# Performance work log

Hardware: AMD Instinct MI355X
Metric: run time of the kernel (lower is better)

The kernel has to match this reference:

```python
import jax, jax.numpy as jnp
import numpy as np

B, T, D = 2, 4096, 1024      # batch, seq, hidden_dim
E, I = 16, 512               # n_routed_experts, expert_intermediate
K = 2                        # n_activated_experts
IS = 2048                    # shared_expert_intermediate
ALPHA = 1e-4                 # balance_loss_alpha
EPS = 1e-9


def setup_inputs() -> dict:
    key = jax.random.key(0)
    ks = jax.random.split(key, 8)
    s = lambda k, shape, fan: jax.random.normal(k, shape, jnp.float32) * (fan ** -0.5)
    return {
        "x": jax.random.normal(ks[0], (B, T, D), jnp.float32),
        "gate_w": s(ks[1], (D, E), D),            # router gate (no bias)
        "expert_bias": jnp.zeros((E,), jnp.float32),
        "sh_gate": s(ks[2], (D, IS), D),          # shared expert SwiGLU
        "sh_up": s(ks[3], (D, IS), D),
        "sh_down": s(ks[4], (IS, D), IS),
        "ex_gate": s(ks[5], (E, D, I), D),        # routed experts (stacked)
        "ex_up": s(ks[6], (E, D, I), D),
        "ex_down": s(ks[7], (E, I, D), I),
    }


def _swiglu(x, wg, wu, wd):
    return (jax.nn.silu(x @ wg) * (x @ wu)) @ wd


def reference(x, gate_w, expert_bias, sh_gate, sh_up, sh_down, ex_gate, ex_up, ex_down):
    Bq, Tq, Dq = x.shape
    # shared expert path (n_shared_experts = 1)
    shared = _swiglu(x, sh_gate, sh_up, sh_down)

    xf = x.reshape(Bq * Tq, Dq)                       # (N, D)
    N = xf.shape[0]

    # --- router: sigmoid gating, bias-adjusted top-k, normalized gates ---
    affinity = jax.nn.sigmoid(xf @ gate_w)            # (N, E)
    scores = affinity + expert_bias[None, :]
    _, idx = jax.lax.top_k(scores, K)                 # (N, K) int
    gv = jnp.take_along_axis(affinity, idx, axis=1)   # (N, K) gathered from affinity
    gv = gv / (gv.sum(-1, keepdims=True) + EPS)

    # --- balance loss (sequence-wise, Eq. 17-20) ---
    expert_mask = jax.nn.one_hot(idx, E, dtype=jnp.float32).sum(1)  # (N, E)
    f = expert_mask.sum(0) * E / (K * N)
    P = (affinity / (affinity.sum(-1, keepdims=True) + EPS)).mean(0)
    balance_loss = ALPHA * (f * P).sum()
    expert_counts = expert_mask.sum(0).astype(jnp.int32)            # (E,)

    # --- dispatch/compute/combine, expressed as dense combine-weight matrix ---
    # w[n, e] = sum of gate values for token n routed to expert e (same math
    # as the masked gather/scatter loop in the original)
    w = jnp.zeros((N, E), jnp.float32).at[jnp.arange(N)[:, None], idx].add(gv)
    h = jax.nn.silu(jnp.einsum('nd,edi->eni', xf, ex_gate)) \
        * jnp.einsum('nd,edi->eni', xf, ex_up)        # (E, N, I)
    routed = jnp.einsum('ne,eni,eid->nd', w, h, ex_down)  # (N, D)
    routed = routed.reshape(Bq, Tq, Dq)

    output = shared + routed  # note: original does NOT add residual despite docstring
    return output, balance_loss, expert_counts
```

## Files before the change

kernel.cpp:

```cpp
#include <hip/hip_runtime.h>
#include <stdint.h>

#define NTOK 8192
#define DDIM 1024
#define NEXP 16
#define KSEL 2
#define ISH 2048
#define IEX 512
#define ALPHAC 1e-4f
#define REPS 1e-9f

typedef __attribute__((ext_vector_type(8))) short short8;
typedef __attribute__((ext_vector_type(4))) float f32x4;

__device__ __forceinline__ unsigned short f2bf(float f){
  union { float f; uint32_t u; } v; v.f = f;
  uint32_t u = v.u;
  uint32_t r = (u + 0x7fffu + ((u >> 16) & 1u)) >> 16;
  return (unsigned short)r;
}
__device__ __forceinline__ float bf2f(unsigned short h){
  union { uint32_t u; float f; } v; v.u = ((uint32_t)h) << 16; return v.f;
}

__device__ __forceinline__ void gload16(const void* g, void* l){
  __builtin_amdgcn_global_load_lds(
      (const __attribute__((address_space(1))) void*)g,
      (__attribute__((address_space(3))) void*)l, 16, 0, 0);
}

template<int RM, int RO>
__global__ __launch_bounds__(256) void transpose_bf16(const float* __restrict__ in,
                                                      unsigned short* __restrict__ outp,
                                                      int R, int C){
  __shared__ float tile[64][65];
  const float* ip = in + (size_t)blockIdx.z * R * C;
  unsigned short* op = outp + (size_t)blockIdx.z * R * C * RM;
  int c0 = blockIdx.x * 64, r0 = blockIdx.y * 64;
  int t = threadIdx.x;
  int tr = t >> 4, tc = (t & 15) * 4;
  #pragma unroll
  for (int i = 0; i < 4; ++i){
    float4 v = *(const float4*)&ip[(size_t)(r0 + tr + i*16) * C + c0 + tc];
    tile[tr + i*16][tc+0] = v.x;
    tile[tr + i*16][tc+1] = v.y;
    tile[tr + i*16][tc+2] = v.z;
    tile[tr + i*16][tc+3] = v.w;
  }
  __syncthreads();
  #pragma unroll
  for (int i = 0; i < 4; ++i){
    int oc = tr + i*16;
    ushort4 w;
    w.x = f2bf(tile[tc+0][oc]);
    w.y = f2bf(tile[tc+1][oc]);
    w.z = f2bf(tile[tc+2][oc]);
    w.w = f2bf(tile[tc+3][oc]);
    *(ushort4*)&op[(size_t)((c0 + oc) * RM + RO) * R + r0 + tc] = w;
  }
}

__global__ __launch_bounds__(256) void logits_kernel(
    const float* __restrict__ x, const float* __restrict__ gw,
    float* __restrict__ logits, unsigned short* __restrict__ xb)
{
  __shared__ float gws[16][1024];
  const int t = threadIdx.x;
  #pragma unroll
  for (int k = 0; k < 16; ++k){
    int idx = t + k * 256;
    float4 v = ((const float4*)gw)[idx];
    int d = idx >> 2, e0 = (idx & 3) * 4;
    gws[e0+0][d] = v.x;
    gws[e0+1][d] = v.y;
    gws[e0+2][d] = v.z;
    gws[e0+3][d] = v.w;
  }
  __syncthreads();
  const int lane = t & 63, w = t >> 6;
  const int nb = blockIdx.x * 16 + w * 4;
  for (int i = 0; i < 4; ++i){
    const int n = nb + i;
    const float4* xr = (const float4*)(x + (size_t)n * DDIM);
    ushort4* xo = (ushort4*)(xb + (size_t)n * DDIM);
    float4 xv[4];
    #pragma unroll
    for (int k = 0; k < 4; ++k) xv[k] = xr[lane + k*64];
    #pragma unroll
    for (int k = 0; k < 4; ++k){
      ushort4 ob;
      ob.x = f2bf(xv[k].x); ob.y = f2bf(xv[k].y);
      ob.z = f2bf(xv[k].z); ob.w = f2bf(xv[k].w);
      xo[lane + k*64] = ob;
    }
    float acc[16];
    #pragma unroll
    for (int e = 0; e < 16; ++e){
      float s = 0.f;
      #pragma unroll
      for (int k = 0; k < 4; ++k){
        float4 g = *(const float4*)&gws[e][(lane + k*64)*4];
        s = fmaf(xv[k].x, g.x, fmaf(xv[k].y, g.y, fmaf(xv[k].z, g.z, fmaf(xv[k].w, g.w, s))));
      }
      acc[e] = s;
    }
    #pragma unroll
    for (int m = 1; m < 64; m <<= 1)
      #pragma unroll
      for (int e = 0; e < 16; ++e)
        acc[e] += __shfl_xor(acc[e], m);
    if (lane == 0){
      float4* op = (float4*)(logits + (size_t)n * 16);
      op[0] = make_float4(acc[0],  acc[1],  acc[2],  acc[3]);
      op[1] = make_float4(acc[4],  acc[5],  acc[6],  acc[7]);
      op[2] = make_float4(acc[8],  acc[9],  acc[10], acc[11]);
      op[3] = make_float4(acc[12], acc[13], acc[14], acc[15]);
    }
  }
}

__global__ __launch_bounds__(256) void router_finish(
    const float* __restrict__ logits, const float* __restrict__ ebias,
    int* __restrict__ idxb, float* __restrict__ gvb,
    float* __restrict__ Ppart, int* __restrict__ Cpart)
{
  __shared__ float Ps[16];
  __shared__ int Cs[16];
  const int t = threadIdx.x;
  if (t < 16){ Ps[t] = 0.f; Cs[t] = 0; }
  __syncthreads();
  const int lane = t & 63;
  const int n = blockIdx.x * 256 + t;
  const float4* lp = (const float4*)(logits + (size_t)n * 16);
  float4 a0 = lp[0], a1 = lp[1], a2 = lp[2], a3 = lp[3];
  float aff[16];
  aff[0]=a0.x; aff[1]=a0.y; aff[2]=a0.z; aff[3]=a0.w;
  aff[4]=a1.x; aff[5]=a1.y; aff[6]=a1.z; aff[7]=a1.w;
  aff[8]=a2.x; aff[9]=a2.y; aff[10]=a2.z; aff[11]=a2.w;
  aff[12]=a3.x; aff[13]=a3.y; aff[14]=a3.z; aff[15]=a3.w;
  float rowsum = REPS;
  #pragma unroll
  for (int e = 0; e < 16; ++e){
    aff[e] = 1.f / (1.f + __expf(-aff[e]));
    rowsum += aff[e];
  }
  float bj[16];
  #pragma unroll
  for (int e = 0; e < 16; ++e) bj[e] = ebias[e];
  float bestS = aff[0] + bj[0], bestA = aff[0]; int i1 = 0;
  #pragma unroll
  for (int j = 1; j < 16; ++j){
    float sc = aff[j] + bj[j];
    bool gt2 = sc > bestS;
    bestS = gt2 ? sc : bestS; bestA = gt2 ? aff[j] : bestA; i1 = gt2 ? j : i1;
  }
  float secS = -1e30f, secA = 0.f; int i2 = 0;
  #pragma unroll
  for (int j = 0; j < 16; ++j){
    float sc = aff[j] + bj[j];
    bool ok = (j != i1) && (sc > secS);
    secS = ok ? sc : secS; secA = ok ? aff[j] : secA; i2 = ok ? j : i2;
  }
  float den = bestA + secA + REPS;
  idxb[n*2]   = i1; idxb[n*2+1] = i2;
  gvb[n*2]    = bestA / den; gvb[n*2+1] = secA / den;

  float inv = 1.f / rowsum;
  float pv[16]; int cv[16];
  #pragma unroll
  for (int e = 0; e < 16; ++e){
    pv[e] = aff[e] * inv;
    cv[e] = (e == i1) + (e == i2);
  }
  #pragma unroll
  for (int m = 1; m < 64; m <<= 1)
    #pragma unroll
    for (int e = 0; e < 16; ++e){
      pv[e] += __shfl_xor(pv[e], m);
      cv[e] += __shfl_xor(cv[e], m);
    }
  if (lane == 0){
    #pragma unroll
    for (int e = 0; e < 16; ++e){
      atomicAdd(&Ps[e], pv[e]);
      atomicAdd(&Cs[e], cv[e]);
    }
  }
  __syncthreads();
  if (t < 16){ Ppart[blockIdx.x*16 + t] = Ps[t]; Cpart[blockIdx.x*16 + t] = Cs[t]; }
}

__global__ __launch_bounds__(256) void finalize2(
    const float* __restrict__ Ppart, const int* __restrict__ Cpart,
    int* __restrict__ counts, int* __restrict__ offs, int* __restrict__ cursor,
    float* __restrict__ out_tail)
{
  __shared__ float P[16];
  __shared__ int C[16];
  int t = threadIdx.x;
  if (t < 16){ P[t] = 0.f; C[t] = 0; }
  __syncthreads();
  if (t < 32){
    int e = t & 15, c = t >> 4;
    float p = 0.f; int cc = 0;
    for (int b = c * 16; b < c * 16 + 16; ++b){ p += Ppart[b*16 + e]; cc += Cpart[b*16 + e]; }
    atomicAdd(&P[e], p); atomicAdd(&C[e], cc);
  }
  __syncthreads();
  if (t == 0){
    int a = 0; float loss = 0.f;
    for (int i = 0; i < 16; ++i){
      offs[i] = a; cursor[i] = a; counts[i] = C[i]; a += C[i];
      loss += ((float)C[i] * (float)NEXP / (float)(KSEL * NTOK)) * (P[i] / (float)NTOK);
      out_tail[1+i] = (float)C[i];
    }
    out_tail[0] = ALPHAC * loss;
  }
}

__global__ __launch_bounds__(256) void slot_assign(
    const int* __restrict__ idxb, const float* __restrict__ gvb,
    int* __restrict__ cursor, int* __restrict__ tokp, float* __restrict__ gatep,
    int* __restrict__ rslot)
{
  int i = blockIdx.x * 256 + threadIdx.x;
  int e = idxb[i];
  int s = atomicAdd(&cursor[e], 1);
  tokp[s] = i >> 1;
  gatep[s] = gvb[i];
  rslot[i] = s;
}

template<bool GROUPED, bool GATHER, int MODE, int NYT>
__global__ __launch_bounds__(256) void gemm128(
    const unsigned short* __restrict__ A,
    const unsigned short* __restrict__ B,
    void* __restrict__ Cout,
    int M, int N, int K,
    const int* __restrict__ counts,
    const int* __restrict__ offsets,
    const int* __restrict__ perm,
    const float* __restrict__ rowscale,
    const unsigned short* __restrict__ yb)
{
  __shared__ __align__(16) unsigned short As[128*64];
  __shared__ __align__(16) unsigned short Bs[128*64];

  const int nwg = gridDim.x;
  const int bid = blockIdx.x;
  const int wg = (bid & 7) * (nwg >> 3) + (bid >> 3);
  const int mtl = wg / NYT;
  const int nt  = wg % NYT;

  int mt = mtl, off = 0, cnt = M;
  const unsigned short* bp = B;
  if (GROUPED){
    int acc_ = 0, e = -1;
    #pragma unroll
    for (int i = 0; i < NEXP; ++i){
      int c = counts[i]; int tt = (c + 127) >> 7;
      if (e < 0 && mtl < acc_ + tt){ e = i; mt = mtl - acc_; off = offsets[i]; cnt = c; }
      acc_ += tt;
    }
    if (e < 0) return;
    bp += (size_t)e * N * K;
  }
  const int m0 = mt * 128, n0 = nt * 128;
  const int t = threadIdx.x;
  const int lane = t & 63;
  const int wid = t >> 6;
  const int wm = (wid >> 1) * 64;
  const int wn = (wid & 1) * 64;
  const int l15 = lane & 15, g = lane >> 4;

  const unsigned short* asrc[4];
  const unsigned short* bsrc[4];
  int ldso[4];
  #pragma unroll
  for (int c = 0; c < 4; ++c){
    int s = (wid*4 + c)*64 + lane;
    int row = s >> 3, c16 = s & 7;
    int scol = (c16 ^ (row & 7)) * 8;
    ldso[c] = (wid*4 + c) * 512;
    int r = m0 + row;
    int rc = GROUPED ? (r < cnt ? r : (cnt > 0 ? cnt - 1 : 0)) : r;
    int ar;
    if (GATHER) ar = perm[off + rc];
    else        ar = GROUPED ? off + rc : rc;
    asrc[c] = A + (size_t)ar * K + scol;
    bsrc[c] = bp + (size_t)(n0 + row) * K + scol;
  }

  f32x4 acc[4][4];
  #pragma unroll
  for (int i = 0; i < 4; ++i)
    #pragma unroll
    for (int j = 0; j < 4; ++j)
      #pragma unroll
      for (int r = 0; r < 4; ++r) acc[i][j][r] = 0.f;

  const int ntk = K >> 6;
  for (int tk = 0; tk < ntk; ++tk){
    const int k0 = tk << 6;
    #pragma unroll
    for (int c = 0; c < 4; ++c) gload16(asrc[c] + k0, (void*)&As[ldso[c]]);
    #pragma unroll
    for (int c = 0; c < 4; ++c) gload16(bsrc[c] + k0, (void*)&Bs[ldso[c]]);
    __syncthreads();
    #pragma unroll
    for (int ks = 0; ks < 2; ++ks){
      short8 af[4], bf[4];
      #pragma unroll
      for (int i = 0; i < 4; ++i){
        int row = wm + i * 16 + l15;
        af[i] = *(const short8*)&As[row * 64 + (((ks*4 + g) ^ (row & 7)) * 8)];
      }
      #pragma unroll
      for (int j = 0; j < 4; ++j){
        int row = wn + j * 16 + l15;
        bf[j] = *(const short8*)&Bs[row * 64 + (((ks*4 + g) ^ (row & 7)) * 8)];
      }
      #pragma unroll
      for (int i = 0; i < 4; ++i)
        #pragma unroll
        for (int j = 0; j < 4; ++j)
          acc[i][j] = __builtin_amdgcn_mfma_f32_16x16x32_bf16(af[i], bf[j], acc[i][j], 0, 0, 0);
    }
    __syncthreads();
  }

  #pragma unroll
  for (int i = 0; i < 4; ++i)
    #pragma unroll
    for (int j = 0; j < 4; ++j)
      #pragma unroll
      for (int r = 0; r < 4; ++r){
        int lr = wm + i * 16 + g * 4 + r;
        int grow = m0 + lr;
        if (GROUPED && grow >= cnt) continue;
        int gcol = n0 + wn + j * 16 + l15;
        size_t orow = GROUPED ? (size_t)(off + grow) : (size_t)grow;
        float val = acc[i][j][r];
        if (MODE == 1){
          ((float*)Cout)[orow * N + gcol] = val;
        } else if (MODE == 2){
          val *= rowscale[off + grow];
          ((unsigned short*)Cout)[orow * N + gcol] = f2bf(val);
        } else if (MODE == 6){
          float uo = __shfl_xor(val, 1);
          if (!(l15 & 1)){
            float rv = val / (1.f + __expf(-val)) * uo;
            ((unsigned short*)Cout)[orow * (N >> 1) + (gcol >> 1)] = f2bf(rv);
          }
        } else if (MODE == 7){
          int s0 = perm[grow*2], s1 = perm[grow*2+1];
          float add = bf2f(yb[(size_t)s0 * N + gcol]) + bf2f(yb[(size_t)s1 * N + gcol]);
          ((float*)Cout)[orow * N + gcol] = val + add;
        }
      }
}

template<int MODE, int NYT>
__global__ __launch_bounds__(512, 1) void gemm256(
    const unsigned short* __restrict__ A,
    const unsigned short* __restrict__ B,
    void* __restrict__ Cout,
    int M, int N, int K)
{
  __shared__ __align__(16) unsigned short As[2][256*64];
  __shared__ __align__(16) unsigned short Bs[2][256*64];

  const int nwg = gridDim.x;
  const int bid = blockIdx.x;
  const int wg = (bid & 7) * (nwg >> 3) + (bid >> 3);
  const int mt  = wg / NYT;
  const int ntc = wg % NYT;

  const int m0 = mt * 256, n0 = ntc * 256;
  const int t = threadIdx.x;
  const int lane = t & 63;
  const int wid = t >> 6;
  const int wm0 = (wid >> 2) * 128;
  const int wn0 = (wid & 3) * 64;
  const int l15 = lane & 15, g = lane >> 4;

  const unsigned short* asrc[4];
  const unsigned short* bsrc[4];
  int ldst[4];
  #pragma unroll
  for (int c = 0; c < 4; ++c){
    int slot = c * 512 + t;
    int row = slot >> 3, c16 = slot & 7;
    int scol = (c16 ^ (row & 7)) * 8;
    ldst[c] = slot * 8;
    asrc[c] = A + (size_t)(m0 + row) * K + scol;
    bsrc[c] = B + (size_t)(n0 + row) * K + scol;
  }

  f32x4 acc[8][4];
  #pragma unroll
  for (int i = 0; i < 8; ++i)
    #pragma unroll
    for (int j = 0; j < 4; ++j)
      #pragma unroll
      for (int r = 0; r < 4; ++r) acc[i][j][r] = 0.f;

  auto STAGE = [&](int buf, int kt){
    const int k0 = kt << 6;
    #pragma unroll
    for (int c = 0; c < 4; ++c) gload16(asrc[c] + k0, (void*)&As[buf][ldst[c]]);
    #pragma unroll
    for (int c = 0; c < 4; ++c) gload16(bsrc[c] + k0, (void*)&Bs[buf][ldst[c]]);
  };

  const int ntk = K >> 6;
  STAGE(0, 0);
  __syncthreads();
  int cur = 0;
  for (int tk = 0; tk < ntk; ++tk){
    if (tk + 1 < ntk) STAGE(cur ^ 1, tk + 1);
    short8 bfr[4][2];
    #pragma unroll
    for (int j = 0; j < 4; ++j)
      #pragma unroll
      for (int ks = 0; ks < 2; ++ks){
        int row = wn0 + j * 16 + l15;
        bfr[j][ks] = *(const short8*)&Bs[cur][row * 64 + (((ks*4 + g) ^ (row & 7)) * 8)];
      }
    #pragma unroll
    for (int mi = 0; mi < 8; ++mi){
      int row = wm0 + mi * 16 + l15;
      short8 af0 = *(const short8*)&As[cur][row * 64 + (((0 + g) ^ (row & 7)) * 8)];
      short8 af1 = *(const short8*)&As[cur][row * 64 + (((4 + g) ^ (row & 7)) * 8)];
      #pragma unroll
      for (int j = 0; j < 4; ++j)
        acc[mi][j] = __builtin_amdgcn_mfma_f32_16x16x32_bf16(af0, bfr[j][0], acc[mi][j], 0, 0, 0);
      #pragma unroll
      for (int j = 0; j < 4; ++j)
        acc[mi][j] = __builtin_amdgcn_mfma_f32_16x16x32_bf16(af1, bfr[j][1], acc[mi][j], 0, 0, 0);
    }
    __syncthreads();
    cur ^= 1;
  }

  #pragma unroll
  for (int mi = 0; mi < 8; ++mi)
    #pragma unroll
    for (int j = 0; j < 4; ++j)
      #pragma unroll
      for (int r = 0; r < 4; ++r){
        int lr = wm0 + mi * 16 + g * 4 + r;
        int grow = m0 + lr;
        int gcol = n0 + wn0 + j * 16 + l15;
        float val = acc[mi][j][r];
        if (MODE == 6){
          float uo = __shfl_xor(val, 1);
          if (!(l15 & 1)){
            float rv = val / (1.f + __expf(-val)) * uo;
            ((unsigned short*)Cout)[(size_t)grow * (N >> 1) + (gcol >> 1)] = f2bf(rv);
          }
        } else {
          ((float*)Cout)[(size_t)grow * N + gcol] = val;
        }
      }
}

extern "C" void kernel_launch(void* const* d_in, const int* in_sizes, int n_in,
                              void* d_out, int out_size, void* d_ws, size_t ws_size,
                              hipStream_t stream)
{
  const float* x       = (const float*)d_in[0];
  const float* gate_w  = (const float*)d_in[1];
  const float* ebias   = (const float*)d_in[2];
  const float* sh_gate = (const float*)d_in[3];
  const float* sh_up   = (const float*)d_in[4];
  const float* sh_down = (const float*)d_in[5];
  const float* ex_gate = (const float*)d_in[6];
  const float* ex_up   = (const float*)d_in[7];
  const float* ex_down = (const float*)d_in[8];
  float* out = (float*)d_out;
  (void)in_sizes; (void)n_in; (void)out_size; (void)ws_size;

  size_t o = 0;
  auto alloc = [&](size_t bytes) -> void* {
    o = (o + 255) & ~(size_t)255;
    void* p = (char*)d_ws + o;
    o += bytes;
    return p;
  };
  unsigned short* xb    = (unsigned short*)alloc((size_t)NTOK*DDIM*2);
  unsigned short* shguT = (unsigned short*)alloc((size_t)2*ISH*DDIM*2);
  unsigned short* shdT  = (unsigned short*)alloc((size_t)DDIM*ISH*2);
  unsigned short* exguT = (unsigned short*)alloc((size_t)NEXP*2*IEX*DDIM*2);
  unsigned short* exdT  = (unsigned short*)alloc((size_t)NEXP*DDIM*IEX*2);
  unsigned short* hbuf  = (unsigned short*)alloc((size_t)NTOK*KSEL*IEX*2);
  unsigned short* big   = (unsigned short*)alloc((size_t)NTOK*ISH*2);
  unsigned short* ybuf  = (unsigned short*)alloc((size_t)NTOK*KSEL*DDIM*2);
  float* logits = (float*)alloc((size_t)NTOK*NEXP*4);
  int*   idxb  = (int*)alloc(NTOK*KSEL*4);
  float* gvb   = (float*)alloc(NTOK*KSEL*4);
  float* Ppart = (float*)alloc(32*16*4);
  int*   Cpart = (int*)alloc(32*16*4);
  int*   counts= (int*)alloc(64);
  int*   offs  = (int*)alloc(64);
  int*   cursor= (int*)alloc(64);
  int*   tokp  = (int*)alloc(NTOK*KSEL*4);
  float* gatep = (float*)alloc(NTOK*KSEL*4);
  int*   rslot = (int*)alloc(NTOK*KSEL*4);

  transpose_bf16<2,0><<<dim3(ISH/64,  DDIM/64, 1),    256, 0, stream>>>(sh_gate, shguT, DDIM, ISH);
  transpose_bf16<2,1><<<dim3(ISH/64,  DDIM/64, 1),    256, 0, stream>>>(sh_up,   shguT, DDIM, ISH);
  transpose_bf16<1,0><<<dim3(DDIM/64, ISH/64,  1),    256, 0, stream>>>(sh_down, shdT, ISH, DDIM);
  transpose_bf16<2,0><<<dim3(IEX/64,  DDIM/64, NEXP), 256, 0, stream>>>(ex_gate, exguT, DDIM, IEX);
  transpose_bf16<2,1><<<dim3(IEX/64,  DDIM/64, NEXP), 256, 0, stream>>>(ex_up,   exguT, DDIM, IEX);
  transpose_bf16<1,0><<<dim3(DDIM/64, IEX/64,  NEXP), 256, 0, stream>>>(ex_down, exdT, IEX, DDIM);

  logits_kernel<<<512, 256, 0, stream>>>(x, gate_w, logits, xb);
  router_finish<<<32, 256, 0, stream>>>(logits, ebias, idxb, gvb, Ppart, Cpart);
  finalize2<<<1, 256, 0, stream>>>(Ppart, Cpart, counts, offs, cursor,
                                   out + (size_t)NTOK*DDIM);
  slot_assign<<<NTOK*KSEL/256, 256, 0, stream>>>(idxb, gvb, cursor, tokp, gatep, rslot);

  gemm128<true,true,6,8><<<144*8, 256, 0, stream>>>(
      xb, exguT, hbuf, 0, 2*IEX, DDIM, counts, offs, tokp, nullptr, nullptr);
  gemm128<true,false,2,8><<<144*8, 256, 0, stream>>>(
      hbuf, exdT, ybuf, 0, DDIM, IEX, counts, offs, nullptr, gatep, nullptr);

  gemm256<6,16><<<32*16, 512, 0, stream>>>(
      xb, shguT, big, NTOK, 2*ISH, DDIM);
  gemm128<false,false,7,8><<<64*8, 256, 0, stream>>>(
      big, shdT, out, NTOK, DDIM, ISH, nullptr, nullptr, rslot, nullptr, ybuf);
}
```

Before: 381.0 us.

## Switch GEMM operands and intermediates from bf16 to fp8 MFMA

Measured after the change: 405.2 us. 1.06x slower.

```diff
diff --git a/kernel.cpp b/kernel.cpp
--- a/kernel.cpp
+++ b/kernel.cpp
@@ -10,7 +10,6 @@
 #define ALPHAC 1e-4f
 #define REPS 1e-9f
 
-typedef __attribute__((ext_vector_type(8))) short short8;
 typedef __attribute__((ext_vector_type(4))) float f32x4;
 
 __device__ __forceinline__ unsigned short f2bf(float f){
@@ -23,6 +22,23 @@
   union { uint32_t u; float f; } v; v.u = ((uint32_t)h) << 16; return v.f;
 }
 
+__device__ __forceinline__ unsigned char f2fp8(float x){
+  union{ float f; uint32_t u; } v; v.f = x;
+  unsigned char sgn = (unsigned char)((v.u >> 31) << 7);
+  uint32_t au = v.u & 0x7fffffffu;
+  if (au >= 0x43E80000u) return sgn | 0x7E;
+  if (au <  0x3A800000u) return sgn;
+  int e  = (int)(au >> 23) - 127;
+  int ee = e < -6 ? -6 : e;
+  float scale = __uint_as_float((uint32_t)(127 + 3 - ee) << 23);
+  int qi = (int)rintf(__uint_as_float(au) * scale);
+  int exp8, man;
+  if (qi >= 16)     { exp8 = ee + 8; man = 0; }
+  else if (qi >= 8) { exp8 = ee + 7; man = qi - 8; }
+  else              { exp8 = 0;      man = qi; }
+  return sgn | (unsigned char)((exp8 << 3) | man);
+}
+
 __device__ __forceinline__ void gload16(const void* g, void* l){
   __builtin_amdgcn_global_load_lds(
       (const __attribute__((address_space(1))) void*)g,
@@ -30,12 +46,12 @@
 }
 
 template<int RM, int RO>
-__global__ __launch_bounds__(256) void transpose_bf16(const float* __restrict__ in,
-                                                      unsigned short* __restrict__ outp,
-                                                      int R, int C){
+__global__ __launch_bounds__(256) void transpose_fp8(const float* __restrict__ in,
+                                                     unsigned char* __restrict__ outp,
+                                                     int R, int C){
   __shared__ float tile[64][65];
   const float* ip = in + (size_t)blockIdx.z * R * C;
-  unsigned short* op = outp + (size_t)blockIdx.z * R * C * RM;
+  unsigned char* op = outp + (size_t)blockIdx.z * R * C * RM;
   int c0 = blockIdx.x * 64, r0 = blockIdx.y * 64;
   int t = threadIdx.x;
   int tr = t >> 4, tc = (t & 15) * 4;
@@ -51,18 +67,18 @@
   #pragma unroll
   for (int i = 0; i < 4; ++i){
     int oc = tr + i*16;
-    ushort4 w;
-    w.x = f2bf(tile[tc+0][oc]);
-    w.y = f2bf(tile[tc+1][oc]);
-    w.z = f2bf(tile[tc+2][oc]);
-    w.w = f2bf(tile[tc+3][oc]);
-    *(ushort4*)&op[(size_t)((c0 + oc) * RM + RO) * R + r0 + tc] = w;
+    uchar4 w;
+    w.x = f2fp8(tile[tc+0][oc]);
+    w.y = f2fp8(tile[tc+1][oc]);
+    w.z = f2fp8(tile[tc+2][oc]);
+    w.w = f2fp8(tile[tc+3][oc]);
+    *(uchar4*)&op[(size_t)((c0 + oc) * RM + RO) * R + r0 + tc] = w;
   }
 }
 
 __global__ __launch_bounds__(256) void logits_kernel(
     const float* __restrict__ x, const float* __restrict__ gw,
-    float* __restrict__ logits, unsigned short* __restrict__ xb)
+    float* __restrict__ logits, unsigned char* __restrict__ xb)
 {
   __shared__ float gws[16][1024];
   const int t = threadIdx.x;
@@ -82,15 +98,15 @@
   for (int i = 0; i < 4; ++i){
     const int n = nb + i;
     const float4* xr = (const float4*)(x + (size_t)n * DDIM);
-    ushort4* xo = (ushort4*)(xb + (size_t)n * DDIM);
+    uchar4* xo = (uchar4*)(xb + (size_t)n * DDIM);
     float4 xv[4];
     #pragma unroll
     for (int k = 0; k < 4; ++k) xv[k] = xr[lane + k*64];
     #pragma unroll
     for (int k = 0; k < 4; ++k){
-      ushort4 ob;
-      ob.x = f2bf(xv[k].x); ob.y = f2bf(xv[k].y);
-      ob.z = f2bf(xv[k].z); ob.w = f2bf(xv[k].w);
+      uchar4 ob;
+      ob.x = f2fp8(xv[k].x); ob.y = f2fp8(xv[k].y);
+      ob.z = f2fp8(xv[k].z); ob.w = f2fp8(xv[k].w);
       xo[lane + k*64] = ob;
     }
     float acc[16];
@@ -233,8 +249,8 @@
 
 template<bool GROUPED, bool GATHER, int MODE, int NYT>
 __global__ __launch_bounds__(256) void gemm128(
-    const unsigned short* __restrict__ A,
-    const unsigned short* __restrict__ B,
+    const unsigned char* __restrict__ A,
+    const unsigned char* __restrict__ B,
     void* __restrict__ Cout,
     int M, int N, int K,
     const int* __restrict__ counts,
@@ -243,8 +259,8 @@
     const float* __restrict__ rowscale,
     const unsigned short* __restrict__ yb)
 {
-  __shared__ __align__(16) unsigned short As[128*64];
-  __shared__ __align__(16) unsigned short Bs[128*64];
+  __shared__ __align__(16) unsigned char As[128*128];
+  __shared__ __align__(16) unsigned char Bs[128*128];
 
   const int nwg = gridDim.x;
   const int bid = blockIdx.x;
@@ -253,7 +269,7 @@
   const int nt  = wg % NYT;
 
   int mt = mtl, off = 0, cnt = M;
-  const unsigned short* bp = B;
+  const unsigned char* bp = B;
   if (GROUPED){
     int acc_ = 0, e = -1;
     #pragma unroll
@@ -273,22 +289,22 @@
   const int wn = (wid & 1) * 64;
   const int l15 = lane & 15, g = lane >> 4;
 
-  const unsigned short* asrc[4];
-  const unsigned short* bsrc[4];
+  const unsigned char* asrc[4];
+  const unsigned char* bsrc[4];
   int ldso[4];
   #pragma unroll
   for (int c = 0; c < 4; ++c){
     int s = (wid*4 + c)*64 + lane;
-    int row = s >> 3, c16 = s & 7;
-    int scol = (c16 ^ (row & 7)) * 8;
-    ldso[c] = (wid*4 + c) * 512;
+    int row = s >> 3, s16 = s & 7;
+    int ssw = (s16 ^ ((row >> 1) & 7)) * 16;
+    ldso[c] = s * 16;
     int r = m0 + row;
     int rc = GROUPED ? (r < cnt ? r : (cnt > 0 ? cnt - 1 : 0)) : r;
     int ar;
     if (GATHER) ar = perm[off + rc];
     else        ar = GROUPED ? off + rc : rc;
-    asrc[c] = A + (size_t)ar * K + scol;
-    bsrc[c] = bp + (size_t)(n0 + row) * K + scol;
+    asrc[c] = A + (size_t)ar * K + ssw;
+    bsrc[c] = bp + (size_t)(n0 + row) * K + ssw;
   }
 
   f32x4 acc[4][4];
@@ -299,32 +315,32 @@
       #pragma unroll
       for (int r = 0; r < 4; ++r) acc[i][j][r] = 0.f;
 
-  const int ntk = K >> 6;
+  const int ntk = K >> 7;
   for (int tk = 0; tk < ntk; ++tk){
-    const int k0 = tk << 6;
+    const int k0 = tk << 7;
     #pragma unroll
     for (int c = 0; c < 4; ++c) gload16(asrc[c] + k0, (void*)&As[ldso[c]]);
     #pragma unroll
     for (int c = 0; c < 4; ++c) gload16(bsrc[c] + k0, (void*)&Bs[ldso[c]]);
     __syncthreads();
     #pragma unroll
-    for (int ks = 0; ks < 2; ++ks){
-      short8 af[4], bf[4];
+    for (int ks = 0; ks < 4; ++ks){
+      long long af[4], bf[4];
       #pragma unroll
       for (int i = 0; i < 4; ++i){
         int row = wm + i * 16 + l15;
-        af[i] = *(const short8*)&As[row * 64 + (((ks*4 + g) ^ (row & 7)) * 8)];
+        af[i] = *(const long long*)&As[row * 128 + (((ks*4 + g) ^ (row & 14)) * 8)];
       }
       #pragma unroll
       for (int j = 0; j < 4; ++j){
         int row = wn + j * 16 + l15;
-        bf[j] = *(const short8*)&Bs[row * 64 + (((ks*4 + g) ^ (row & 7)) * 8)];
+        bf[j] = *(const long long*)&Bs[row * 128 + (((ks*4 + g) ^ (row & 14)) * 8)];
       }
       #pragma unroll
       for (int i = 0; i < 4; ++i)
         #pragma unroll
         for (int j = 0; j < 4; ++j)
-          acc[i][j] = __builtin_amdgcn_mfma_f32_16x16x32_bf16(af[i], bf[j], acc[i][j], 0, 0, 0);
+          acc[i][j] = __builtin_amdgcn_mfma_f32_16x16x32_fp8_fp8(af[i], bf[j], acc[i][j], 0, 0, 0);
     }
     __syncthreads();
   }
@@ -350,7 +366,7 @@
           float uo = __shfl_xor(val, 1);
           if (!(l15 & 1)){
             float rv = val / (1.f + __expf(-val)) * uo;
-            ((unsigned short*)Cout)[orow * (N >> 1) + (gcol >> 1)] = f2bf(rv);
+            ((unsigned char*)Cout)[orow * (N >> 1) + (gcol >> 1)] = f2fp8(rv);
           }
         } else if (MODE == 7){
           int s0 = perm[grow*2], s1 = perm[grow*2+1];
@@ -362,13 +378,13 @@
 
 template<int MODE, int NYT>
 __global__ __launch_bounds__(512, 1) void gemm256(
-    const unsigned short* __restrict__ A,
-    const unsigned short* __restrict__ B,
+    const unsigned char* __restrict__ A,
+    const unsigned char* __restrict__ B,
     void* __restrict__ Cout,
     int M, int N, int K)
 {
-  __shared__ __align__(16) unsigned short As[2][256*64];
-  __shared__ __align__(16) unsigned short Bs[2][256*64];
+  __shared__ __align__(16) unsigned char As[2][256*128];
+  __shared__ __align__(16) unsigned char Bs[2][256*128];
 
   const int nwg = gridDim.x;
   const int bid = blockIdx.x;
@@ -384,17 +400,17 @@
   const int wn0 = (wid & 3) * 64;
   const int l15 = lane & 15, g = lane >> 4;
 
-  const unsigned short* asrc[4];
-  const unsigned short* bsrc[4];
+  const unsigned char* asrc[4];
+  const unsigned char* bsrc[4];
   int ldst[4];
   #pragma unroll
   for (int c = 0; c < 4; ++c){
     int slot = c * 512 + t;
-    int row = slot >> 3, c16 = slot & 7;
-    int scol = (c16 ^ (row & 7)) * 8;
-    ldst[c] = slot * 8;
-    asrc[c] = A + (size_t)(m0 + row) * K + scol;
-    bsrc[c] = B + (size_t)(n0 + row) * K + scol;
+    int row = slot >> 3, s16 = slot & 7;
+    int ssw = (s16 ^ ((row >> 1) & 7)) * 16;
+    ldst[c] = slot * 16;
+    asrc[c] = A + (size_t)(m0 + row) * K + ssw;
+    bsrc[c] = B + (size_t)(n0 + row) * K + ssw;
   }
 
   f32x4 acc[8][4];
@@ -406,38 +422,39 @@
       for (int r = 0; r < 4; ++r) acc[i][j][r] = 0.f;
 
   auto STAGE = [&](int buf, int kt){
-    const int k0 = kt << 6;
+    const int k0 = kt << 7;
     #pragma unroll
     for (int c = 0; c < 4; ++c) gload16(asrc[c] + k0, (void*)&As[buf][ldst[c]]);
     #pragma unroll
     for (int c = 0; c < 4; ++c) gload16(bsrc[c] + k0, (void*)&Bs[buf][ldst[c]]);
   };
 
-  const int ntk = K >> 6;
+  const int ntk = K >> 7;
   STAGE(0, 0);
   __syncthreads();
   int cur = 0;
   for (int tk = 0; tk < ntk; ++tk){
     if (tk + 1 < ntk) STAGE(cur ^ 1, tk + 1);
-    short8 bfr[4][2];
+    long long bfr[4][4];
     #pragma unroll
     for (int j = 0; j < 4; ++j)
       #pragma unroll
-      for (int ks = 0; ks < 2; ++ks){
+      for (int ks = 0; ks < 4; ++ks){
         int row = wn0 + j * 16 + l15;
-        bfr[j][ks] = *(const short8*)&Bs[cur][row * 64 + (((ks*4 + g) ^ (row & 7)) * 8)];
+        bfr[j][ks] = *(const long long*)&Bs[cur][row * 128 + (((ks*4 + g) ^ (row & 14)) * 8)];
       }
     #pragma unroll
     for (int mi = 0; mi < 8; ++mi){
       int row = wm0 + mi * 16 + l15;
-      short8 af0 = *(const short8*)&As[cur][row * 64 + (((0 + g) ^ (row & 7)) * 8)];
-      short8 af1 = *(const short8*)&As[cur][row * 64 + (((4 + g) ^ (row & 7)) * 8)];
-      #pragma unroll
-      for (int j = 0; j < 4; ++j)
-        acc[mi][j] = __builtin_amdgcn_mfma_f32_16x16x32_bf16(af0, bfr[j][0], acc[mi][j], 0, 0, 0);
-      #pragma unroll
-      for (int j = 0; j < 4; ++j)
-        acc[mi][j] = __builtin_amdgcn_mfma_f32_16x16x32_bf16(af1, bfr[j][1], acc[mi][j], 0, 0, 0);
+      long long af[4];
+      #pragma unroll
+      for (int ks = 0; ks < 4; ++ks)
+        af[ks] = *(const long long*)&As[cur][row * 128 + (((ks*4 + g) ^ (row & 14)) * 8)];
+      #pragma unroll
+      for (int ks = 0; ks < 4; ++ks)
+        #pragma unroll
+        for (int j = 0; j < 4; ++j)
+          acc[mi][j] = __builtin_amdgcn_mfma_f32_16x16x32_fp8_fp8(af[ks], bfr[j][ks], acc[mi][j], 0, 0, 0);
     }
     __syncthreads();
     cur ^= 1;
@@ -457,7 +474,7 @@
           float uo = __shfl_xor(val, 1);
           if (!(l15 & 1)){
             float rv = val / (1.f + __expf(-val)) * uo;
-            ((unsigned short*)Cout)[(size_t)grow * (N >> 1) + (gcol >> 1)] = f2bf(rv);
+            ((unsigned char*)Cout)[(size_t)grow * (N >> 1) + (gcol >> 1)] = f2fp8(rv);
           }
         } else {
           ((float*)Cout)[(size_t)grow * N + gcol] = val;
@@ -488,14 +505,14 @@
     o += bytes;
     return p;
   };
-  unsigned short* xb    = (unsigned short*)alloc((size_t)NTOK*DDIM*2);
-  unsigned short* shguT = (unsigned short*)alloc((size_t)2*ISH*DDIM*2);
-  unsigned short* shdT  = (unsigned short*)alloc((size_t)DDIM*ISH*2);
-  unsigned short* exguT = (unsigned short*)alloc((size_t)NEXP*2*IEX*DDIM*2);
-  unsigned short* exdT  = (unsigned short*)alloc((size_t)NEXP*DDIM*IEX*2);
-  unsigned short* hbuf  = (unsigned short*)alloc((size_t)NTOK*KSEL*IEX*2);
-  unsigned short* big   = (unsigned short*)alloc((size_t)NTOK*ISH*2);
-  unsigned short* ybuf  = (unsigned short*)alloc((size_t)NTOK*KSEL*DDIM*2);
+  unsigned char* xb    = (unsigned char*)alloc((size_t)NTOK*DDIM);
+  unsigned char* shguT = (unsigned char*)alloc((size_t)2*ISH*DDIM);
+  unsigned char* shdT  = (unsigned char*)alloc((size_t)DDIM*ISH);
+  unsigned char* exguT = (unsigned char*)alloc((size_t)NEXP*2*IEX*DDIM);
+  unsigned char* exdT  = (unsigned char*)alloc((size_t)NEXP*DDIM*IEX);
+  unsigned char* hbuf  = (unsigned char*)alloc((size_t)NTOK*KSEL*IEX);
+  unsigned char* big   = (unsigned char*)alloc((size_t)NTOK*ISH);
+  unsigned short* ybuf = (unsigned short*)alloc((size_t)NTOK*KSEL*DDIM*2);
   float* logits = (float*)alloc((size_t)NTOK*NEXP*4);
   int*   idxb  = (int*)alloc(NTOK*KSEL*4);
   float* gvb   = (float*)alloc(NTOK*KSEL*4);
@@ -508,12 +525,12 @@
   float* gatep = (float*)alloc(NTOK*KSEL*4);
   int*   rslot = (int*)alloc(NTOK*KSEL*4);
 
-  transpose_bf16<2,0><<<dim3(ISH/64,  DDIM/64, 1),    256, 0, stream>>>(sh_gate, shguT, DDIM, ISH);
-  transpose_bf16<2,1><<<dim3(ISH/64,  DDIM/64, 1),    256, 0, stream>>>(sh_up,   shguT, DDIM, ISH);
-  transpose_bf16<1,0><<<dim3(DDIM/64, ISH/64,  1),    256, 0, stream>>>(sh_down, shdT, ISH, DDIM);
-  transpose_bf16<2,0><<<dim3(IEX/64,  DDIM/64, NEXP), 256, 0, stream>>>(ex_gate, exguT, DDIM, IEX);
-  transpose_bf16<2,1><<<dim3(IEX/64,  DDIM/64, NEXP), 256, 0, stream>>>(ex_up,   exguT, DDIM, IEX);
-  transpose_bf16<1,0><<<dim3(DDIM/64, IEX/64,  NEXP), 256, 0, stream>>>(ex_down, exdT, IEX, DDIM);
+  transpose_fp8<2,0><<<dim3(ISH/64,  DDIM/64, 1),    256, 0, stream>>>(sh_gate, shguT, DDIM, ISH);
+  transpose_fp8<2,1><<<dim3(ISH/64,  DDIM/64, 1),    256, 0, stream>>>(sh_up,   shguT, DDIM, ISH);
+  transpose_fp8<1,0><<<dim3(DDIM/64, ISH/64,  1),    256, 0, stream>>>(sh_down, shdT, ISH, DDIM);
+  transpose_fp8<2,0><<<dim3(IEX/64,  DDIM/64, NEXP), 256, 0, stream>>>(ex_gate, exguT, DDIM, IEX);
+  transpose_fp8<2,1><<<dim3(IEX/64,  DDIM/64, NEXP), 256, 0, stream>>>(ex_up,   exguT, DDIM, IEX);
+  transpose_fp8<1,0><<<dim3(DDIM/64, IEX/64,  NEXP), 256, 0, stream>>>(ex_down, exdT, IEX, DDIM);
 
   logits_kernel<<<512, 256, 0, stream>>>(x, gate_w, logits, xb);
   router_finish<<<32, 256, 0, stream>>>(logits, ebias, idxb, gvb, Ppart, Cpart);
```
